# Optimization experiments

Hardware: AMD Instinct MI355X
Metric: run time of the kernel (lower is better)

## Reference

```python
import jax, jax.numpy as jnp
import numpy as np

S, B, H = 2048, 2, 2048
NH = 16
HD = H // NH
SCALE = HD ** -0.5


def setup_inputs() -> dict:
    key = jax.random.key(0)
    ks = jax.random.split(key, 5)
    sigma = 0.02
    return {
        "x": jax.random.normal(ks[0], (S, B, H), dtype=jnp.float32),
        "wq": jax.random.normal(ks[1], (H, H), dtype=jnp.float32) * sigma,
        "wk": jax.random.normal(ks[2], (H, H), dtype=jnp.float32) * sigma,
        "wv": jax.random.normal(ks[3], (H, H), dtype=jnp.float32) * sigma,
        "wo": jax.random.normal(ks[4], (H, H), dtype=jnp.float32) * sigma,
    }


def reference(x, wq, wk, wv, wo):
    # x: [s, b, h]; F.linear(x, W) == x @ W.T
    q = x @ wq.T
    k = x @ wk.T
    v = x @ wv.T
    s, b, _ = q.shape
    # [s, b, h] -> [b, nh, s, hd]
    def split_heads(t):
        return t.reshape(s, b, NH, HD).transpose(1, 2, 0, 3)
    q, k, v = split_heads(q), split_heads(k), split_heads(v)
    scores = jnp.einsum("bhqd,bhkd->bhqk", q, k) * SCALE
    attn = jax.nn.softmax(scores.astype(jnp.float32), axis=-1).astype(q.dtype)
    out = jnp.einsum("bhqk,bhkd->bhqd", attn, v)
    # [b, nh, s, hd] -> [s, b, h]
    out = out.transpose(2, 0, 1, 3).reshape(s, b, NH * HD)
    return out @ wo.T
```

## Files before the change

### kernel.cpp

```cpp
#include <hip/hip_runtime.h>

typedef __bf16 bf16;
typedef __bf16 bf16x8 __attribute__((ext_vector_type(8)));
typedef float f32x4 __attribute__((ext_vector_type(4)));
typedef float f32x16 __attribute__((ext_vector_type(16)));
typedef unsigned int uint;
typedef uint uint2v __attribute__((ext_vector_type(2)));

#define GLOAD16(g, l)                                                        \
  __builtin_amdgcn_global_load_lds(                                          \
      (const __attribute__((address_space(1))) void*)(g),                    \
      (__attribute__((address_space(3))) void*)(l), 16, 0, 0)

__device__ inline uint pack_bf16(float a, float b) {
  union { bf16 h[2]; uint u; } x;
  x.h[0] = (bf16)a; x.h[1] = (bf16)b;
  return x.u;
}

__global__ void cast_f32_to_bf16(const float* __restrict__ in,
                                 bf16* __restrict__ out, int n8, float scale) {
  int i = blockIdx.x * blockDim.x + threadIdx.x;
  if (i >= n8) return;
  const float4* p = reinterpret_cast<const float4*>(in) + (size_t)i * 2;
  float4 a = p[0], b = p[1];
  bf16x8 o;
  o[0] = (bf16)(a.x * scale); o[1] = (bf16)(a.y * scale);
  o[2] = (bf16)(a.z * scale); o[3] = (bf16)(a.w * scale);
  o[4] = (bf16)(b.x * scale); o[5] = (bf16)(b.y * scale);
  o[6] = (bf16)(b.z * scale); o[7] = (bf16)(b.w * scale);
  *reinterpret_cast<bf16x8*>(out + (size_t)i * 8) = o;
}

__global__ void cast4(const float* __restrict__ x, const float* __restrict__ wq,
                      const float* __restrict__ wk, const float* __restrict__ wv,
                      bf16* __restrict__ xb, bf16* __restrict__ wqk,
                      bf16* __restrict__ wvb, float qscale) {
  int i = blockIdx.x * blockDim.x + threadIdx.x;
  const float* src;
  bf16* dst;
  float s = 1.0f;
  int j;
  if (i < 1048576) {
    src = x; dst = xb; j = i;
  } else {
    int k = i - 1048576;
    int r = k >> 19;
    j = k & 524287;
    src = r == 0 ? wq : r == 1 ? wk : wv;
    dst = r == 0 ? wqk : r == 1 ? wqk + 4194304 : wvb;
    s = r == 0 ? qscale : 1.0f;
  }
  const float4* p = reinterpret_cast<const float4*>(src) + (size_t)j * 2;
  float4 a = p[0], b = p[1];
  bf16x8 o;
  o[0] = (bf16)(a.x * s); o[1] = (bf16)(a.y * s);
  o[2] = (bf16)(a.z * s); o[3] = (bf16)(a.w * s);
  o[4] = (bf16)(b.x * s); o[5] = (bf16)(b.y * s);
  o[6] = (bf16)(b.z * s); o[7] = (bf16)(b.w * s);
  *reinterpret_cast<bf16x8*>(dst + (size_t)j * 8) = o;
}

template <typename OT>
__global__ __launch_bounds__(512, 1) void gemm_nt_256sq(
    const bf16* __restrict__ A, const bf16* __restrict__ B, OT* __restrict__ C,
    int K, int lda, int ldb, int ldc, long cSplit) {
  extern __shared__ char sh[];
  const int t = threadIdx.x;
  const int w = t >> 6, lane = t & 63;
  const int l15 = lane & 15, l4 = lane >> 4;
  const int wr = w >> 2, wc = w & 3;
  const int gx = gridDim.x, gy = gridDim.y;
  const int nwg = gx * gy;
  const int bid = blockIdx.y * gx + blockIdx.x;
  const int fid = (bid & 7) * (nwg >> 3) + (bid >> 3);
  const int by = fid / gx, bx = fid - by * gx;
  const int m0 = by * 256, n0 = bx * 256;
  OT* Cg = C + ((n0 & 2048) ? cSplit : 0);

  int sRow[4], sCol[4];
#pragma unroll
  for (int i = 0; i < 4; i++) {
    int sB_ = (i * 512 + t) * 16;
    int row = sB_ >> 7;
    int ge = (sB_ ^ ((row & 7) << 4)) >> 1;
    sRow[i] = ge >> 6;
    sCol[i] = ge & 63;
  }

  const int NT = K >> 6;
  f32x4 acc[8][4] = {};

  auto stage = [&](int tt) {
    char* dst = sh + (size_t)(tt & 1) * 65536;
    const int k0 = tt * 64;
#pragma unroll
    for (int i = 0; i < 4; i++)
      GLOAD16(A + (size_t)(m0 + sRow[i]) * lda + k0 + sCol[i],
              dst + (i * 512 + w * 64) * 16);
#pragma unroll
    for (int i = 0; i < 4; i++)
      GLOAD16(B + (size_t)(n0 + sRow[i]) * ldb + k0 + sCol[i],
              dst + 32768 + (i * 512 + w * 64) * 16);
  };

  stage(0);
  for (int tt = 0; tt < NT; ++tt) {
    asm volatile("s_waitcnt vmcnt(0)" ::: "memory");
    __builtin_amdgcn_s_barrier();

    const char* Ab = sh + (size_t)(tt & 1) * 65536;
    const char* Bb = Ab + 32768;
    bf16x8 bfr[4][2];
#pragma unroll
    for (int n = 0; n < 4; n++)
#pragma unroll
      for (int kk = 0; kk < 2; kk++) {
        int row = wc * 64 + n * 16 + l15;
        int off = (row * 128 + kk * 64 + l4 * 16) ^ ((row & 7) << 4);
        bfr[n][kk] = *reinterpret_cast<const bf16x8*>(Bb + off);
      }
#pragma unroll
    for (int mp = 0; mp < 4; mp++) {
      bf16x8 af[2][2];
#pragma unroll
      for (int m = 0; m < 2; m++)
#pragma unroll
        for (int kk = 0; kk < 2; kk++) {
          int row = wr * 128 + (mp * 2 + m) * 16 + l15;
          int off = (row * 128 + kk * 64 + l4 * 16) ^ ((row & 7) << 4);
          af[m][kk] = *reinterpret_cast<const bf16x8*>(Ab + off);
        }
      __builtin_amdgcn_s_setprio(1);
#pragma unroll
      for (int m = 0; m < 2; m++)
#pragma unroll
        for (int n = 0; n < 4; n++)
#pragma unroll
          for (int kk = 0; kk < 2; kk++)
            acc[mp * 2 + m][n] = __builtin_amdgcn_mfma_f32_16x16x32_bf16(
                af[m][kk], bfr[n][kk], acc[mp * 2 + m][n], 0, 0, 0);
      __builtin_amdgcn_s_setprio(0);
      if (mp == 0 && tt + 1 < NT) stage(tt + 1);
    }
  }

#pragma unroll
  for (int m = 0; m < 8; m++)
#pragma unroll
    for (int n = 0; n < 4; n++)
#pragma unroll
      for (int j = 0; j < 4; j++) {
        int row = m0 + wr * 128 + m * 16 + l4 * 4 + j;
        int col = n0 + wc * 64 + n * 16 + l15;
        Cg[(size_t)row * ldc + col] = (OT)acc[m][n][j];
      }
}

template <typename OT>
__global__ __launch_bounds__(512, 2) void gemm_nt_256(
    const bf16* __restrict__ A, const bf16* __restrict__ B, OT* __restrict__ C,
    int K, int lda, int ldb, int ldc, long bsB, long bsC, long cSplit) {
  extern __shared__ char sh[];
  const int t = threadIdx.x;
  const int w = t >> 6, lane = t & 63;
  const int l15 = lane & 15, l4 = lane >> 4;
  const int wr = w >> 1, wc = w & 1;
  const int gx = gridDim.x, gy = gridDim.y;
  const int nwg = gx * gy;
  const int bid = blockIdx.y * gx + blockIdx.x;
  const int fid = (bid & 7) * (nwg >> 3) + (bid >> 3);
  const int by = fid / gx, bx = fid - by * gx;
  const int m0 = by * 256;
  const int n0 = bx * 128;
  const bf16* Bg = B + (size_t)blockIdx.z * bsB;
  OT* Cg = C + (size_t)blockIdx.z * bsC + ((n0 & 2048) ? cSplit : 0);

  int sRow[4], sCol[4];
#pragma unroll
  for (int i = 0; i < 4; i++) {
    int sB_ = (i * 512 + t) * 16;
    int row = sB_ >> 7;
    int ge = (sB_ ^ ((row & 7) << 4)) >> 1;
    sRow[i] = ge >> 6;
    sCol[i] = ge & 63;
  }

  const int NT = K >> 6;
  f32x4 acc[4][4] = {};

  auto stage = [&](int tt) {
    char* dst = sh + (size_t)(tt % 3) * 49152;
    const int k0 = tt * 64;
#pragma unroll
    for (int i = 0; i < 4; i++)
      GLOAD16(A + (size_t)(m0 + sRow[i]) * lda + k0 + sCol[i],
              dst + (i * 512 + w * 64) * 16);
#pragma unroll
    for (int i = 0; i < 2; i++)
      GLOAD16(Bg + (size_t)(n0 + sRow[i]) * ldb + k0 + sCol[i],
              dst + 32768 + (i * 512 + w * 64) * 16);
  };

  stage(0);
  stage(1);
  for (int tt = 0; tt < NT; ++tt) {
    if (tt < NT - 1)
      asm volatile("s_waitcnt vmcnt(6)" ::: "memory");
    else
      asm volatile("s_waitcnt vmcnt(0)" ::: "memory");
    __builtin_amdgcn_s_barrier();

    const char* Ab = sh + (size_t)(tt % 3) * 49152;
    const char* Bb = Ab + 32768;
    bf16x8 bfr[4][2];
#pragma unroll
    for (int n = 0; n < 4; n++)
#pragma unroll
      for (int kk = 0; kk < 2; kk++) {
        int row = wc * 64 + n * 16 + l15;
        int off = (row * 128 + kk * 64 + l4 * 16) ^ ((row & 7) << 4);
        bfr[n][kk] = *reinterpret_cast<const bf16x8*>(Bb + off);
      }
    bf16x8 af0[2][2];
#pragma unroll
    for (int m = 0; m < 2; m++)
#pragma unroll
      for (int kk = 0; kk < 2; kk++) {
        int row = wr * 64 + m * 16 + l15;
        int off = (row * 128 + kk * 64 + l4 * 16) ^ ((row & 7) << 4);
        af0[m][kk] = *reinterpret_cast<const bf16x8*>(Ab + off);
      }
    __builtin_amdgcn_s_setprio(1);
#pragma unroll
    for (int m = 0; m < 2; m++)
#pragma unroll
      for (int n = 0; n < 4; n++)
#pragma unroll
        for (int kk = 0; kk < 2; kk++)
          acc[m][n] = __builtin_amdgcn_mfma_f32_16x16x32_bf16(
              af0[m][kk], bfr[n][kk], acc[m][n], 0, 0, 0);
    __builtin_amdgcn_s_setprio(0);

    if (tt + 2 < NT) stage(tt + 2);

    bf16x8 af1[2][2];
#pragma unroll
    for (int m = 0; m < 2; m++)
#pragma unroll
      for (int kk = 0; kk < 2; kk++) {
        int row = wr * 64 + (2 + m) * 16 + l15;
        int off = (row * 128 + kk * 64 + l4 * 16) ^ ((row & 7) << 4);
        af1[m][kk] = *reinterpret_cast<const bf16x8*>(Ab + off);
      }
    __builtin_amdgcn_s_setprio(1);
#pragma unroll
    for (int m = 0; m < 2; m++)
#pragma unroll
      for (int n = 0; n < 4; n++)
#pragma unroll
        for (int kk = 0; kk < 2; kk++)
          acc[2 + m][n] = __builtin_amdgcn_mfma_f32_16x16x32_bf16(
              af1[m][kk], bfr[n][kk], acc[2 + m][n], 0, 0, 0);
    __builtin_amdgcn_s_setprio(0);
  }

#pragma unroll
  for (int m = 0; m < 4; m++)
#pragma unroll
    for (int n = 0; n < 4; n++)
#pragma unroll
      for (int j = 0; j < 4; j++) {
        int row = m0 + wr * 64 + m * 16 + l4 * 4 + j;
        int col = n0 + wc * 64 + n * 16 + l15;
        Cg[(size_t)row * ldc + col] = (OT)acc[m][n][j];
      }
}

__global__ __launch_bounds__(512, 2) void attn_fwd(
    const bf16* __restrict__ Q, const bf16* __restrict__ Kb,
    const bf16* __restrict__ Vt, bf16* __restrict__ O) {
  extern __shared__ char ash[];
  const int t = threadIdx.x, w = t >> 6, lane = t & 63;
  const int l31 = lane & 31, half = lane >> 5;
  const int bh = blockIdx.x;
  const int b = bh >> 4, h = bh & 15;
  const int sq0 = blockIdx.y * 256 + w * 32;
  const size_t hoff = (size_t)h * 128;
  const size_t bO = (size_t)b * 2048 + hoff;

  bf16x8 qf[8];
  {
    const bf16* qp = Q + ((size_t)(sq0 + l31) * 2 + b) * 2048 + hoff + half * 8;
#pragma unroll
    for (int dc = 0; dc < 8; dc++)
      qf[dc] = *reinterpret_cast<const bf16x8*>(qp + dc * 16);
  }

  const bf16* kp[2];
  const bf16* vp[2];
#pragma unroll
  for (int i = 0; i < 2; i++) {
    int s = i * 512 + t;
    int row = s >> 4, g = s & 15;
    int lg = g ^ (row & 15);
    kp[i] = Kb + ((size_t)row * 2 + b) * 2048 + hoff + lg * 8;
    int d = row * 2 + (lg >> 3);
    vp[i] = Vt + (bO + d) * 2048 + (lg & 7) * 8;
  }

  auto stage = [&](int slot, int sk0) {
    char* Kd = ash + (size_t)slot * 32768;
    char* Vd = Kd + 16384;
#pragma unroll
    for (int i = 0; i < 2; i++)
      GLOAD16(kp[i] + (size_t)sk0 * 4096, Kd + (i * 512 + w * 64) * 16);
#pragma unroll
    for (int i = 0; i < 2; i++)
      GLOAD16(vp[i] + sk0, Vd + (i * 512 + w * 64) * 16);
  };

  f32x16 acc_o[4] = {};
  float m_run = -3e38f, l_run = 0.f;

  stage(0, 0);
  stage(1, 64);

  for (int it = 0; it < 32; ++it) {
    if (it < 31)
      asm volatile("s_waitcnt vmcnt(4)" ::: "memory");
    else
      asm volatile("s_waitcnt vmcnt(0)" ::: "memory");
    __builtin_amdgcn_s_barrier();

    const char* ksb = ash + (size_t)(it % 3) * 32768;
    const char* vsb = ksb + 16384;

    f32x16 sc[2] = {};
    bf16x8 ka[4], kb_[4], kc[4];
    auto loadK = [&](bf16x8 (&dst)[4], int g) {
#pragma unroll
      for (int j = 0; j < 2; j++) {
        int dc = g * 2 + j;
        int kx = ((dc * 2 + half) ^ (l31 & 15)) << 4;
        dst[j * 2 + 0] = *reinterpret_cast<const bf16x8*>(ksb + (l31 << 8) + kx);
        dst[j * 2 + 1] =
            *reinterpret_cast<const bf16x8*>(ksb + ((32 + l31) << 8) + kx);
      }
    };
    auto mfmaK = [&](bf16x8 (&kf)[4], int g) {
#pragma unroll
      for (int j = 0; j < 2; j++) {
        sc[0] = __builtin_amdgcn_mfma_f32_32x32x16_bf16(kf[j * 2 + 0],
                                                        qf[g * 2 + j], sc[0], 0, 0, 0);
        sc[1] = __builtin_amdgcn_mfma_f32_32x32x16_bf16(kf[j * 2 + 1],
                                                        qf[g * 2 + j], sc[1], 0, 0, 0);
      }
    };
    loadK(ka, 0);
    loadK(kb_, 1);
    loadK(kc, 2);
    __builtin_amdgcn_s_setprio(1);
    mfmaK(ka, 0);
    loadK(ka, 3);
    mfmaK(kb_, 1);
    mfmaK(kc, 2);
    mfmaK(ka, 3);
    __builtin_amdgcn_s_setprio(0);

    if (it + 2 < 32) stage((it + 2) % 3, (it + 2) * 64);

    float red[8];
#pragma unroll
    for (int r = 0; r < 8; r++)
      red[r] = fmaxf(fmaxf(sc[0][r], sc[0][r + 8]),
                     fmaxf(sc[1][r], sc[1][r + 8]));
#pragma unroll
    for (int s = 4; s >= 1; s >>= 1)
#pragma unroll
      for (int r = 0; r < s; r++) red[r] = fmaxf(red[r], red[r + s]);
    float pmax = fmaxf(red[0], __shfl_xor(red[0], 32));

    if (!__all(pmax - m_run <= 11.0f)) {
      float mn = fmaxf(m_run, pmax);
      float f = exp2f(m_run - mn);
      m_run = mn;
      l_run *= f;
#pragma unroll
      for (int idx = 0; idx < 16; idx++) {
        float fr = __shfl(f, (idx & 3) + 8 * (idx >> 2) + half * 4);
#pragma unroll
        for (int dcb = 0; dcb < 4; dcb++) acc_o[dcb][idx] *= fr;
      }
    }

#pragma unroll
    for (int kt = 0; kt < 2; kt++)
#pragma unroll
      for (int r = 0; r < 16; r++) sc[kt][r] = exp2f(sc[kt][r] - m_run);
#pragma unroll
    for (int r = 0; r < 8; r++)
      red[r] = (sc[0][r] + sc[0][r + 8]) + (sc[1][r] + sc[1][r + 8]);
#pragma unroll
    for (int s = 4; s >= 1; s >>= 1)
#pragma unroll
      for (int r = 0; r < s; r++) red[r] += red[r + s];
    l_run += red[0] + __shfl_xor(red[0], 32);

    bf16x8 va[4], vb[4], vc[4];
    auto loadV = [&](bf16x8 (&dst)[4], int dcb) {
      int rp = dcb * 16 + (l31 >> 1);
      int pbit = (l31 & 1) << 3;
#pragma unroll
      for (int skc = 0; skc < 4; skc++)
        dst[skc] = *reinterpret_cast<const bf16x8*>(
            vsb + (rp << 8) + (((pbit + skc * 2 + half) ^ (l31 >> 1)) << 4));
    };
    loadV(va, 0);
    loadV(vb, 1);
    loadV(vc, 2);

    uint pa[4][4];
#pragma unroll
    for (int skc = 0; skc < 4; skc++) {
      int kt = skc >> 1, s8 = (skc & 1) * 8;
      uint pk01 = pack_bf16(sc[kt][s8 + 0], sc[kt][s8 + 1]);
      uint pk23 = pack_bf16(sc[kt][s8 + 2], sc[kt][s8 + 3]);
      uint pk45 = pack_bf16(sc[kt][s8 + 4], sc[kt][s8 + 5]);
      uint pk67 = pack_bf16(sc[kt][s8 + 6], sc[kt][s8 + 7]);
      uint2v r02 = __builtin_amdgcn_permlane32_swap(pk01, pk45, false, false);
      uint2v r13 = __builtin_amdgcn_permlane32_swap(pk23, pk67, false, false);
      pa[skc][0] = r02[0];
      pa[skc][1] = r13[0];
      pa[skc][2] = r02[1];
      pa[skc][3] = r13[1];
    }

    auto mfmaV = [&](bf16x8 (&vf)[4], int dcb) {
#pragma unroll
      for (int skc = 0; skc < 4; skc++) {
        union { uint u[4]; bf16x8 v; } af;
        af.u[0] = pa[skc][0]; af.u[1] = pa[skc][1];
        af.u[2] = pa[skc][2]; af.u[3] = pa[skc][3];
        acc_o[dcb] = __builtin_amdgcn_mfma_f32_32x32x16_bf16(
            af.v, vf[skc], acc_o[dcb], 0, 0, 0);
      }
    };
    __builtin_amdgcn_s_setprio(1);
    mfmaV(va, 0);
    loadV(va, 3);
    mfmaV(vb, 1);
    mfmaV(vc, 2);
    mfmaV(va, 3);
    __builtin_amdgcn_s_setprio(0);
  }

  float inv = 1.0f / l_run;
#pragma unroll
  for (int idx = 0; idx < 16; idx++) {
    int sr = (idx & 3) + 8 * (idx >> 2) + half * 4;
    float invr = __shfl(inv, sr);
    bf16* op = O + ((size_t)(sq0 + sr) * 2 + b) * 2048 + hoff + l31;
#pragma unroll
    for (int dcb = 0; dcb < 4; dcb++)
      op[dcb * 32] = (bf16)(acc_o[dcb][idx] * invr);
  }
}

extern "C" void kernel_launch(void* const* d_in, const int* in_sizes, int n_in,
                              void* d_out, int out_size, void* d_ws,
                              size_t ws_size, hipStream_t stream) {
  (void)in_sizes; (void)n_in; (void)out_size; (void)ws_size;
  const float* x  = (const float*)d_in[0];
  const float* wq = (const float*)d_in[1];
  const float* wk = (const float*)d_in[2];
  const float* wv = (const float*)d_in[3];
  const float* wo = (const float*)d_in[4];
  float* out = (float*)d_out;
  char* ws = (char*)d_ws;
  bf16* xb   = (bf16*)(ws);
  bf16* qb   = (bf16*)(ws + (1u << 24));
  bf16* kb   = (bf16*)(ws + (2u << 24));
  bf16* vt   = (bf16*)(ws + (3u << 24));
  bf16* wb   = (bf16*)(ws + (4u << 24));
  bf16* wqk  = vt;
  bf16* attn = xb;
  const float SCALE = 0.08838834764831845f * 1.4426950408889634f;
  const int SMEM = 3 * 49152;
  const int SMEM_QK = 2 * 65536;
  const int SMEM_A = 3 * 32768;
  const long CSPLIT = (long)(kb - qb) - 2048;

  hipFuncSetAttribute((const void*)gemm_nt_256sq<bf16>,
                      hipFuncAttributeMaxDynamicSharedMemorySize, SMEM_QK);
  hipFuncSetAttribute((const void*)gemm_nt_256<bf16>,
                      hipFuncAttributeMaxDynamicSharedMemorySize, SMEM);
  hipFuncSetAttribute((const void*)gemm_nt_256<float>,
                      hipFuncAttributeMaxDynamicSharedMemorySize, SMEM);
  hipFuncSetAttribute((const void*)attn_fwd,
                      hipFuncAttributeMaxDynamicSharedMemorySize, SMEM_A);

  cast4<<<10240, 256, 0, stream>>>(x, wq, wk, wv, xb, wqk, wb, SCALE);

  dim3 gqk(16, 16, 1);
  gemm_nt_256sq<bf16><<<gqk, 512, SMEM_QK, stream>>>(xb, wqk, qb, 2048, 2048,
                                                     2048, 2048, CSPLIT);

  dim3 g2(16, 8, 2);
  gemm_nt_256<bf16><<<g2, 512, SMEM, stream>>>(wb, xb, vt, 2048, 2048, 4096, 2048,
                                               2048L, 4194304L, 0);

  dim3 ga(32, 8);
  attn_fwd<<<ga, 512, SMEM_A, stream>>>(qb, kb, vt, attn);

  cast_f32_to_bf16<<<2048, 256, 0, stream>>>(wo, wb, 4194304 / 8, 1.0f);
  dim3 g1(16, 16, 1);
  gemm_nt_256<float><<<g1, 512, SMEM, stream>>>(attn, wb, out, 2048, 2048, 2048,
                                                2048, 0, 0, 0);
}
```

Measured before the change: 245.4 us.

## Software-pipeline QK^T one tile ahead of softmax and PV in attention loop

Restructures the flash-attention main loop so the QK^T scores for key tile it+1 are computed while the softmax and PV product for tile it are processed. The score MFMAs can then overlap the exp/reduction VALU work, reducing dependency stalls. The cost is an extra set of score accumulators (more VGPRs, possibly lower occupancy) and a full vmcnt(0) wait every iteration, which replaces the earlier partial wait and may expose load latency.

```diff
diff --git a/kernel.cpp b/kernel.cpp
--- a/kernel.cpp
+++ b/kernel.cpp
@@ -320,61 +320,85 @@
       GLOAD16(vp[i] + sk0, Vd + (i * 512 + w * 64) * 16);
   };
 
+  auto loadK = [&](const char* ksb, bf16x8 (&dst)[4], int g) {
+#pragma unroll
+    for (int j = 0; j < 2; j++) {
+      int dc = g * 2 + j;
+      int kx = ((dc * 2 + half) ^ (l31 & 15)) << 4;
+      dst[j * 2 + 0] = *reinterpret_cast<const bf16x8*>(ksb + (l31 << 8) + kx);
+      dst[j * 2 + 1] =
+          *reinterpret_cast<const bf16x8*>(ksb + ((32 + l31) << 8) + kx);
+    }
+  };
+
   f32x16 acc_o[4] = {};
   float m_run = -3e38f, l_run = 0.f;
 
   stage(0, 0);
   stage(1, 64);
-
-  for (int it = 0; it < 32; ++it) {
-    if (it < 31)
-      asm volatile("s_waitcnt vmcnt(4)" ::: "memory");
-    else
-      asm volatile("s_waitcnt vmcnt(0)" ::: "memory");
-    __builtin_amdgcn_s_barrier();
-
-    const char* ksb = ash + (size_t)(it % 3) * 32768;
-    const char* vsb = ksb + 16384;
-
-    f32x16 sc[2] = {};
+  asm volatile("s_waitcnt vmcnt(4)" ::: "memory");
+  __builtin_amdgcn_s_barrier();
+
+  f32x16 scA[2] = {};
+  {
+    const char* ksb = ash;
     bf16x8 ka[4], kb_[4], kc[4];
-    auto loadK = [&](bf16x8 (&dst)[4], int g) {
+    auto mfmaK = [&](bf16x8 (&kf)[4], int g) {
 #pragma unroll
       for (int j = 0; j < 2; j++) {
-        int dc = g * 2 + j;
-        int kx = ((dc * 2 + half) ^ (l31 & 15)) << 4;
-        dst[j * 2 + 0] = *reinterpret_cast<const bf16x8*>(ksb + (l31 << 8) + kx);
-        dst[j * 2 + 1] =
-            *reinterpret_cast<const bf16x8*>(ksb + ((32 + l31) << 8) + kx);
+        scA[0] = __builtin_amdgcn_mfma_f32_32x32x16_bf16(
+            kf[j * 2 + 0], qf[g * 2 + j], scA[0], 0, 0, 0);
+        scA[1] = __builtin_amdgcn_mfma_f32_32x32x16_bf16(
+            kf[j * 2 + 1], qf[g * 2 + j], scA[1], 0, 0, 0);
       }
     };
-    auto mfmaK = [&](bf16x8 (&kf)[4], int g) {
-#pragma unroll
-      for (int j = 0; j < 2; j++) {
-        sc[0] = __builtin_amdgcn_mfma_f32_32x32x16_bf16(kf[j * 2 + 0],
-                                                        qf[g * 2 + j], sc[0], 0, 0, 0);
-        sc[1] = __builtin_amdgcn_mfma_f32_32x32x16_bf16(kf[j * 2 + 1],
-                                                        qf[g * 2 + j], sc[1], 0, 0, 0);
-      }
-    };
-    loadK(ka, 0);
-    loadK(kb_, 1);
-    loadK(kc, 2);
+    loadK(ksb, ka, 0);
+    loadK(ksb, kb_, 1);
+    loadK(ksb, kc, 2);
     __builtin_amdgcn_s_setprio(1);
     mfmaK(ka, 0);
-    loadK(ka, 3);
+    loadK(ksb, ka, 3);
     mfmaK(kb_, 1);
     mfmaK(kc, 2);
     mfmaK(ka, 3);
     __builtin_amdgcn_s_setprio(0);
-
+  }
+
+  for (int it = 0; it < 32; ++it) {
+    asm volatile("s_waitcnt vmcnt(0)" ::: "memory");
+    __builtin_amdgcn_s_barrier();
     if (it + 2 < 32) stage((it + 2) % 3, (it + 2) * 64);
 
+    f32x16 scB[2] = {};
+    if (it + 1 < 32) {
+      const char* ksb = ash + (size_t)((it + 1) % 3) * 32768;
+      bf16x8 ka[4], kb_[4], kc[4];
+      auto mfmaK = [&](bf16x8 (&kf)[4], int g) {
+#pragma unroll
+        for (int j = 0; j < 2; j++) {
+          scB[0] = __builtin_amdgcn_mfma_f32_32x32x16_bf16(
+              kf[j * 2 + 0], qf[g * 2 + j], scB[0], 0, 0, 0);
+          scB[1] = __builtin_amdgcn_mfma_f32_32x32x16_bf16(
+              kf[j * 2 + 1], qf[g * 2 + j], scB[1], 0, 0, 0);
+        }
+      };
+      loadK(ksb, ka, 0);
+      loadK(ksb, kb_, 1);
+      loadK(ksb, kc, 2);
+      __builtin_amdgcn_s_setprio(1);
+      mfmaK(ka, 0);
+      loadK(ksb, ka, 3);
+      mfmaK(kb_, 1);
+      mfmaK(kc, 2);
+      mfmaK(ka, 3);
+      __builtin_amdgcn_s_setprio(0);
+    }
+
     float red[8];
 #pragma unroll
     for (int r = 0; r < 8; r++)
-      red[r] = fmaxf(fmaxf(sc[0][r], sc[0][r + 8]),
-                     fmaxf(sc[1][r], sc[1][r + 8]));
+      red[r] = fmaxf(fmaxf(scA[0][r], scA[0][r + 8]),
+                     fmaxf(scA[1][r], scA[1][r + 8]));
 #pragma unroll
     for (int s = 4; s >= 1; s >>= 1)
 #pragma unroll
@@ -397,16 +421,17 @@
 #pragma unroll
     for (int kt = 0; kt < 2; kt++)
 #pragma unroll
-      for (int r = 0; r < 16; r++) sc[kt][r] = exp2f(sc[kt][r] - m_run);
+      for (int r = 0; r < 16; r++) scA[kt][r] = exp2f(scA[kt][r] - m_run);
 #pragma unroll
     for (int r = 0; r < 8; r++)
-      red[r] = (sc[0][r] + sc[0][r + 8]) + (sc[1][r] + sc[1][r + 8]);
+      red[r] = (scA[0][r] + scA[0][r + 8]) + (scA[1][r] + scA[1][r + 8]);
 #pragma unroll
     for (int s = 4; s >= 1; s >>= 1)
 #pragma unroll
       for (int r = 0; r < s; r++) red[r] += red[r + s];
     l_run += red[0] + __shfl_xor(red[0], 32);
 
+    const char* vsb = ash + (size_t)(it % 3) * 32768 + 16384;
     bf16x8 va[4], vb[4], vc[4];
     auto loadV = [&](bf16x8 (&dst)[4], int dcb) {
       int rp = dcb * 16 + (l31 >> 1);
@@ -424,10 +449,10 @@
 #pragma unroll
     for (int skc = 0; skc < 4; skc++) {
       int kt = skc >> 1, s8 = (skc & 1) * 8;
-      uint pk01 = pack_bf16(sc[kt][s8 + 0], sc[kt][s8 + 1]);
-      uint pk23 = pack_bf16(sc[kt][s8 + 2], sc[kt][s8 + 3]);
-      uint pk45 = pack_bf16(sc[kt][s8 + 4], sc[kt][s8 + 5]);
-      uint pk67 = pack_bf16(sc[kt][s8 + 6], sc[kt][s8 + 7]);
+      uint pk01 = pack_bf16(scA[kt][s8 + 0], scA[kt][s8 + 1]);
+      uint pk23 = pack_bf16(scA[kt][s8 + 2], scA[kt][s8 + 3]);
+      uint pk45 = pack_bf16(scA[kt][s8 + 4], scA[kt][s8 + 5]);
+      uint pk67 = pack_bf16(scA[kt][s8 + 6], scA[kt][s8 + 7]);
       uint2v r02 = __builtin_amdgcn_permlane32_swap(pk01, pk45, false, false);
       uint2v r13 = __builtin_amdgcn_permlane32_swap(pk23, pk67, false, false);
       pa[skc][0] = r02[0];
@@ -453,6 +478,9 @@
     mfmaV(vc, 2);
     mfmaV(va, 3);
     __builtin_amdgcn_s_setprio(0);
+
+    scA[0] = scB[0];
+    scA[1] = scB[1];
   }
 
   float inv = 1.0f / l_run;
```

Result: no change. 245.3 us (-0.0%).
